# Kernel tuning notes

Measured on AMD Instinct MI355X. Metric: run time of the kernel, lower is better.

## Reference

```python
import jax, jax.numpy as jnp
import numpy as np

N = 100000
IN_CH = 1024
Z = 32
E = 1600000


def _gcn_conv(x, src, dst, W, b, n_nodes):
    # PyG GCNConv: add self-loops, symmetric deg^{-1/2} normalization,
    # message = norm * (x @ W)[src], scatter-add into dst, plus bias.
    loop = jnp.arange(n_nodes)
    s = jnp.concatenate([src, loop])
    d = jnp.concatenate([dst, loop])
    deg = jax.ops.segment_sum(jnp.ones_like(s, dtype=x.dtype), d, num_segments=n_nodes)
    dinv = jnp.where(deg > 0, jax.lax.rsqrt(deg), 0.0)
    norm = dinv[s] * dinv[d]                     # [E+N]
    h = x @ W                                    # [N, out]
    msg = h[s] * norm[:, None]                   # [E+N, out]
    out = jax.ops.segment_sum(msg, d, num_segments=n_nodes)
    return out + b


def setup_inputs() -> dict:
    key = jax.random.key(0)
    ks = jax.random.split(key, 10)
    x = jax.random.normal(ks[0], (N, IN_CH), dtype=jnp.float32)
    edge_index = jax.random.randint(ks[1], (2, E), 0, N, dtype=jnp.int64)
    def lin(k, fan_in, fan_out):
        bound = 1.0 / np.sqrt(fan_in)
        kw, kb = jax.random.split(k)
        W = jax.random.uniform(kw, (fan_in, fan_out), jnp.float32, -bound, bound)
        b = jax.random.uniform(kb, (fan_out,), jnp.float32, -bound, bound)
        return W, b
    Wg1, bg1 = lin(ks[2], IN_CH, 2 * Z)
    Wg2, bg2 = lin(ks[3], 2 * Z, Z)
    Wf1, bf1 = lin(ks[4], Z, 2 * Z)
    Wf2, bf2 = lin(ks[5], 2 * Z, IN_CH)
    return {"x": x, "edge_index": edge_index,
            "Wg1": Wg1, "bg1": bg1, "Wg2": Wg2, "bg2": bg2,
            "Wf1": Wf1, "bf1": bf1, "Wf2": Wf2, "bf2": bf2}


def reference(x, edge_index, Wg1, bg1, Wg2, bg2, Wf1, bf1, Wf2, bf2):
    src, dst = edge_index[0], edge_index[1]
    h = jax.nn.relu(_gcn_conv(x, src, dst, Wg1, bg1, N))
    z = _gcn_conv(h, src, dst, Wg2, bg2, N)          # encode output
    d = jax.nn.relu(z @ Wf1 + bf1)
    out = jax.nn.relu(d @ Wf2 + bf2)                 # decode output
    return out
```

## Files before the change

### kernel.cpp

```cpp
#include <hip/hip_runtime.h>

#define NN 100000
#define EE 1600000

using bf16x8 = __attribute__((ext_vector_type(8))) short;
using f32x4  = __attribute__((ext_vector_type(4))) float;

static __device__ __forceinline__ unsigned short f2bh(float f) {
    unsigned int u = __float_as_uint(f);
    return (unsigned short)((u + 0x7FFFu + ((u >> 16) & 1u)) >> 16);
}
static __device__ __forceinline__ float bh2f(unsigned short h) {
    return __uint_as_float(((unsigned int)h) << 16);
}

static __device__ __forceinline__ void split_pack(float4 a, float4 b,
                                                  bf16x8& h, bf16x8& l) {
    float f[8] = {a.x, a.y, a.z, a.w, b.x, b.y, b.z, b.w};
    union { bf16x8 v; unsigned int u[4]; } H, L;
    #pragma unroll
    for (int e = 0; e < 4; ++e) {
        unsigned int u0 = __float_as_uint(f[2 * e]);
        unsigned int u1 = __float_as_uint(f[2 * e + 1]);
        H.u[e] = (u0 >> 16) | (u1 & 0xFFFF0000u);
        float r0 = f[2 * e]     - __uint_as_float(u0 & 0xFFFF0000u);
        float r1 = f[2 * e + 1] - __uint_as_float(u1 & 0xFFFF0000u);
        L.u[e] = (__float_as_uint(r0) >> 16) | (__float_as_uint(r1) & 0xFFFF0000u);
    }
    h = H.v; l = L.v;
}

__global__ __launch_bounds__(256) void k_init(unsigned int* cursor) {
    int v = blockIdx.x * 256 + threadIdx.x;
    if (v < NN) cursor[v] = 0u;
}

__global__ __launch_bounds__(256) void k_fill(const int* __restrict__ src,
        const int* __restrict__ dst, unsigned int* cursor, int* __restrict__ bkt) {
    int e = blockIdx.x * 256 + threadIdx.x;
    if (e < EE) {
        int d = dst[e];
        unsigned int pos = atomicAdd(&cursor[d], 1u);
        bkt[(size_t)d * 64 + pos] = src[e];
    }
}

__global__ __launch_bounds__(256) void k_dinv(const unsigned int* __restrict__ deg, float* dinv) {
    int v = blockIdx.x * 256 + threadIdx.x;
    if (v < NN) dinv[v] = rsqrtf((float)(deg[v] + 1u));
}

__global__ __launch_bounds__(256) void k_prepW1(const float* __restrict__ W,
        unsigned short* __restrict__ img) {
    int t = blockIdx.x * 256 + threadIdx.x;
    int k = t >> 6, c = t & 63;
    float f = W[k * 64 + c];
    unsigned short h = f2bh(f);
    int chunk = k >> 5, kk = k & 31;
    size_t base = (size_t)chunk * 4608 + (size_t)c * 36 + kk;
    img[base] = h;
    img[base + 2304] = f2bh(f - bh2f(h));
}

__global__ __launch_bounds__(256) void k_prepW2(const float* __restrict__ W,
        unsigned short* __restrict__ wh, unsigned short* __restrict__ wl) {
    int t = blockIdx.x * 256 + threadIdx.x;
    int k = t >> 10, c = t & 1023;
    float f = W[k * 1024 + c];
    unsigned short h = f2bh(f);
    wh[c * 64 + k] = h;
    wl[c * 64 + k] = f2bh(f - bh2f(h));
}

__global__ __launch_bounds__(256) void k_gemm1(const float* __restrict__ x,
        const unsigned short* __restrict__ wimg,
        const float* __restrict__ dinv, float* __restrict__ g1) {
    __shared__ __align__(16) unsigned short bs[2][2][64][36];
    const int tid = threadIdx.x;
    const int lane = tid & 63, w = tid >> 6;
    const int l16 = lane & 15, g = lane >> 4;
    const int row0 = blockIdx.x * 64;
    const int rA = row0 + w * 16 + l16;
    const bool okA = rA < NN;
    const float* xp = x + (size_t)rA * 1024 + g * 8;
    const char* wb = (const char*)wimg;
    f32x4 acc[4] = {};
    for (int j = w; j < 9; j += 4)
        __builtin_amdgcn_global_load_lds((const unsigned int*)(wb + j * 1024 + lane * 16),
                                         (unsigned int*)((char*)&bs[0][0][0][0] + j * 1024), 16, 0, 0);
    float4 xr0 = make_float4(0.f,0.f,0.f,0.f), xr1 = xr0;
    if (okA) { xr0 = *(const float4*)(xp); xr1 = *(const float4*)(xp + 4); }
    __syncthreads();
    int cur = 0;
    for (int t = 0; t < 32; ++t) {
        float4 nx0 = make_float4(0.f,0.f,0.f,0.f), nx1 = nx0;
        if (t < 31) {
            const char* gb = wb + (size_t)(t + 1) * 9216;
            char* lb = (char*)&bs[cur ^ 1][0][0][0];
            for (int j = w; j < 9; j += 4)
                __builtin_amdgcn_global_load_lds((const unsigned int*)(gb + j * 1024 + lane * 16),
                                                 (unsigned int*)(lb + j * 1024), 16, 0, 0);
            if (okA) { nx0 = *(const float4*)(xp + (t + 1) * 32);
                       nx1 = *(const float4*)(xp + (t + 1) * 32 + 4); }
        }
        bf16x8 ah, al;
        split_pack(xr0, xr1, ah, al);
        #pragma unroll
        for (int nf = 0; nf < 4; ++nf) {
            bf16x8 bh = *(const bf16x8*)&bs[cur][0][nf * 16 + l16][g * 8];
            bf16x8 bl = *(const bf16x8*)&bs[cur][1][nf * 16 + l16][g * 8];
            acc[nf] = __builtin_amdgcn_mfma_f32_16x16x32_bf16(ah, bh, acc[nf], 0, 0, 0);
            acc[nf] = __builtin_amdgcn_mfma_f32_16x16x32_bf16(al, bh, acc[nf], 0, 0, 0);
            acc[nf] = __builtin_amdgcn_mfma_f32_16x16x32_bf16(ah, bl, acc[nf], 0, 0, 0);
        }
        __syncthreads();
        xr0 = nx0; xr1 = nx1; cur ^= 1;
    }
    #pragma unroll
    for (int r = 0; r < 4; ++r) {
        int node = row0 + w * 16 + g * 4 + r;
        if (node < NN) {
            float di = dinv[node];
            #pragma unroll
            for (int nf = 0; nf < 4; ++nf)
                g1[(size_t)node * 64 + nf * 16 + l16] = acc[nf][r] * di;
        }
    }
}

__global__ __launch_bounds__(256) void k_gather64(const float* __restrict__ g1,
        const int* __restrict__ bkt, const unsigned int* __restrict__ deg,
        const float* __restrict__ dinv, const float* __restrict__ bg1,
        float* __restrict__ h) {
    int wv = (blockIdx.x * 256 + threadIdx.x) >> 6;
    int lane = threadIdx.x & 63;
    if (wv >= NN) return;
    unsigned int n = deg[wv];
    const int* b = bkt + (size_t)wv * 64;
    float sum = g1[(size_t)wv * 64 + lane];
    unsigned int i = 0;
    for (; i + 4 <= n; i += 4) {
        int s0 = b[i], s1 = b[i + 1], s2 = b[i + 2], s3 = b[i + 3];
        float v0 = g1[(size_t)s0 * 64 + lane];
        float v1 = g1[(size_t)s1 * 64 + lane];
        float v2 = g1[(size_t)s2 * 64 + lane];
        float v3 = g1[(size_t)s3 * 64 + lane];
        sum += (v0 + v1) + (v2 + v3);
    }
    for (; i < n; ++i) sum += g1[(size_t)b[i] * 64 + lane];
    h[(size_t)wv * 64 + lane] = fmaxf(sum * dinv[wv] + bg1[lane], 0.f);
}

__global__ __launch_bounds__(256) void k_layer2(const float* __restrict__ h,
        const float* __restrict__ Wg2, const float* __restrict__ dinv,
        float* __restrict__ g2) {
    __shared__ __align__(16) float as[64][68];
    __shared__ __align__(16) float wsh[64][32];
    const int tid = threadIdx.x;
    const int node0 = blockIdx.x * 64;
    {
        const int lr = tid >> 4, lk = (tid & 15) * 4;
        #pragma unroll
        for (int l = 0; l < 4; ++l) {
            int r = lr + l * 16, v = node0 + r;
            float4 a = make_float4(0.f, 0.f, 0.f, 0.f);
            if (v < NN) a = *(const float4*)(h + (size_t)v * 64 + lk);
            *(float4*)&as[r][lk] = a;
        }
        const int wr = tid >> 3, wk = (tid & 7) * 4;
        #pragma unroll
        for (int l = 0; l < 2; ++l) {
            int r = wr + l * 32;
            *(float4*)&wsh[r][wk] = *(const float4*)(Wg2 + (size_t)r * 32 + wk);
        }
    }
    __syncthreads();
    const int tx = tid & 7, ty = tid >> 3;
    float acc[2][4] = {{0.f}};
    for (int kk = 0; kk < 64; kk += 4) {
        float wv[4][4];
        #pragma unroll
        for (int j = 0; j < 4; ++j)
            *(float4*)&wv[j][0] = *(const float4*)&wsh[kk + j][tx * 4];
        #pragma unroll
        for (int i = 0; i < 2; ++i) {
            float xv[4];
            *(float4*)&xv[0] = *(const float4*)&as[ty * 2 + i][kk];
            #pragma unroll
            for (int j = 0; j < 4; ++j) {
                #pragma unroll
                for (int c = 0; c < 4; ++c)
                    acc[i][c] += xv[j] * wv[j][c];
            }
        }
    }
    #pragma unroll
    for (int i = 0; i < 2; ++i) {
        int v = node0 + ty * 2 + i;
        if (v < NN) {
            float di = dinv[v];
            float4 o;
            o.x = acc[i][0] * di; o.y = acc[i][1] * di;
            o.z = acc[i][2] * di; o.w = acc[i][3] * di;
            *(float4*)(g2 + (size_t)v * 32 + tx * 4) = o;
        }
    }
}

__global__ __launch_bounds__(256) void k_gather32(const float* __restrict__ g2,
        const int* __restrict__ bkt, const unsigned int* __restrict__ deg,
        const float* __restrict__ dinv, const float* __restrict__ bg2,
        float* __restrict__ z) {
    int node = (blockIdx.x * 256 + threadIdx.x) >> 5;
    int c = threadIdx.x & 31;
    if (node >= NN) return;
    unsigned int n = deg[node];
    const int* b = bkt + (size_t)node * 64;
    float sum = g2[(size_t)node * 32 + c];
    unsigned int i = 0;
    for (; i + 4 <= n; i += 4) {
        int s0 = b[i], s1 = b[i + 1], s2 = b[i + 2], s3 = b[i + 3];
        float v0 = g2[(size_t)s0 * 32 + c];
        float v1 = g2[(size_t)s1 * 32 + c];
        float v2 = g2[(size_t)s2 * 32 + c];
        float v3 = g2[(size_t)s3 * 32 + c];
        sum += (v0 + v1) + (v2 + v3);
    }
    for (; i < n; ++i) sum += g2[(size_t)b[i] * 32 + c];
    z[(size_t)node * 32 + c] = sum * dinv[node] + bg2[c];
}

__global__ __launch_bounds__(256) void k_decode(const float* __restrict__ z,
        const float* __restrict__ Wf1, const float* __restrict__ bf1,
        const unsigned short* __restrict__ w2hg, const unsigned short* __restrict__ w2lg,
        const float* __restrict__ bf2, float* __restrict__ out) {
    __shared__ __align__(16) unsigned char smem[35328];
    float (*dsh)[68] = (float (*)[68])smem;
    float (*zs)[36]  = (float (*)[36])(smem + 17408);
    float (*w1s)[64] = (float (*)[64])(smem + 26624);
    unsigned short (*w2h)[72] = (unsigned short (*)[72])smem;
    unsigned short (*w2l)[72] = (unsigned short (*)[72])(smem + 9216);
    float (*ost)[66] = (float (*)[66])(smem + 18432);
    const int tid = threadIdx.x;
    const int lane = tid & 63, w = tid >> 6;
    const int l16 = lane & 15, g = lane >> 4;
    const int node0 = blockIdx.x * 64;

    uint4 ph[2], pl[2];
    #pragma unroll
    for (int j = 0; j < 2; ++j) {
        int fi = tid + 256 * j;
        int c = fi >> 3, k8 = (fi & 7) * 8;
        ph[j] = *(const uint4*)(w2hg + (size_t)c * 64 + k8);
        pl[j] = *(const uint4*)(w2lg + (size_t)c * 64 + k8);
    }

    #pragma unroll
    for (int j = 0; j < 2; ++j) {
        int fi = tid + 256 * j;
        int v = fi >> 3, m4 = (fi & 7) * 4;
        float4 zz = make_float4(0.f, 0.f, 0.f, 0.f);
        if (node0 + v < NN) zz = *(const float4*)(z + (size_t)(node0 + v) * 32 + m4);
        *(float4*)&zs[v][m4] = zz;
    }
    #pragma unroll
    for (int j = 0; j < 2; ++j) {
        int fi = tid + 256 * j;
        int r = fi >> 4, c4 = (fi & 15) * 4;
        *(float4*)&w1s[r][c4] = *(const float4*)(Wf1 + (size_t)r * 64 + c4);
    }
    __syncthreads();

    {
        const int dtx = tid & 15, dty = tid >> 4;
        float acc[4][4] = {{0.f}};
        for (int m = 0; m < 32; m += 4) {
            float wv[4][4];
            #pragma unroll
            for (int j = 0; j < 4; ++j)
                *(float4*)&wv[j][0] = *(const float4*)&w1s[m + j][dtx * 4];
            #pragma unroll
            for (int i = 0; i < 4; ++i) {
                float zv[4];
                *(float4*)&zv[0] = *(const float4*)&zs[dty * 4 + i][m];
                #pragma unroll
                for (int j = 0; j < 4; ++j) {
                    #pragma unroll
                    for (int c = 0; c < 4; ++c)
                        acc[i][c] += zv[j] * wv[j][c];
                }
            }
        }
        float4 b4 = *(const float4*)(bf1 + dtx * 4);
        #pragma unroll
        for (int i = 0; i < 4; ++i) {
            float4 dd;
            dd.x = fmaxf(acc[i][0] + b4.x, 0.f);
            dd.y = fmaxf(acc[i][1] + b4.y, 0.f);
            dd.z = fmaxf(acc[i][2] + b4.z, 0.f);
            dd.w = fmaxf(acc[i][3] + b4.w, 0.f);
            *(float4*)&dsh[dty * 4 + i][dtx * 4] = dd;
        }
    }
    __syncthreads();

    bf16x8 ah[2], al[2];
    {
        int row = w * 16 + l16;
        #pragma unroll
        for (int s = 0; s < 2; ++s) {
            int k0 = s * 32 + g * 8;
            float4 f0 = *(float4*)&dsh[row][k0];
            float4 f1 = *(float4*)&dsh[row][k0 + 4];
            float fv[8] = {f0.x, f0.y, f0.z, f0.w, f1.x, f1.y, f1.z, f1.w};
            bf16x8 hv, lv;
            #pragma unroll
            for (int e = 0; e < 8; ++e) {
                unsigned short hh = f2bh(fv[e]);
                hv[e] = (short)hh;
                lv[e] = (short)f2bh(fv[e] - bh2f(hh));
            }
            ah[s] = hv; al[s] = lv;
        }
    }
    __syncthreads();

    #pragma unroll
    for (int j = 0; j < 2; ++j) {
        int fi = tid + 256 * j;
        int c = fi >> 3, k8 = (fi & 7) * 8;
        *(uint4*)&w2h[c][k8] = ph[j];
        *(uint4*)&w2l[c][k8] = pl[j];
        ph[j] = *(const uint4*)(w2hg + (size_t)(64 + c) * 64 + k8);
        pl[j] = *(const uint4*)(w2lg + (size_t)(64 + c) * 64 + k8);
    }
    __syncthreads();

    for (int ch = 0; ch < 16; ++ch) {
        const int col0 = ch * 64;
        f32x4 acc[4] = {};
        #pragma unroll
        for (int nf = 0; nf < 4; ++nf) {
            int c = nf * 16 + l16;
            #pragma unroll
            for (int s = 0; s < 2; ++s) {
                int k0 = s * 32 + g * 8;
                bf16x8 bh = *(const bf16x8*)&w2h[c][k0];
                bf16x8 bl = *(const bf16x8*)&w2l[c][k0];
                acc[nf] = __builtin_amdgcn_mfma_f32_16x16x32_bf16(ah[s], bh, acc[nf], 0, 0, 0);
                acc[nf] = __builtin_amdgcn_mfma_f32_16x16x32_bf16(al[s], bh, acc[nf], 0, 0, 0);
                acc[nf] = __builtin_amdgcn_mfma_f32_16x16x32_bf16(ah[s], bl, acc[nf], 0, 0, 0);
            }
        }
        #pragma unroll
        for (int nf = 0; nf < 4; ++nf) {
            float b = bf2[col0 + nf * 16 + l16];
            #pragma unroll
            for (int r = 0; r < 4; ++r)
                ost[w * 16 + g * 4 + r][nf * 16 + l16] = fmaxf(acc[nf][r] + b, 0.f);
        }
        __syncthreads();
        if (ch < 15) {
            #pragma unroll
            for (int j = 0; j < 2; ++j) {
                int fi = tid + 256 * j;
                int c = fi >> 3, k8 = (fi & 7) * 8;
                *(uint4*)&w2h[c][k8] = ph[j];
                *(uint4*)&w2l[c][k8] = pl[j];
                if (ch < 14) {
                    ph[j] = *(const uint4*)(w2hg + (size_t)((ch + 2) * 64 + c) * 64 + k8);
                    pl[j] = *(const uint4*)(w2lg + (size_t)((ch + 2) * 64 + c) * 64 + k8);
                }
            }
        }
        #pragma unroll
        for (int j = 0; j < 4; ++j) {
            int fi = tid + 256 * j;
            int row = fi >> 4, c4 = (fi & 15) * 4;
            int node = node0 + row;
            if (node < NN) {
                float4 o = *(float4*)&ost[row][c4];
                *(float4*)(out + (size_t)node * 1024 + col0 + c4) = o;
            }
        }
        __syncthreads();
    }
}

extern "C" void kernel_launch(void* const* d_in, const int* in_sizes, int n_in,
                              void* d_out, int out_size, void* d_ws, size_t ws_size,
                              hipStream_t stream) {
    const float* x   = (const float*)d_in[0];
    const int* ei    = (const int*)d_in[1];
    const float* Wg1 = (const float*)d_in[2];
    const float* bg1 = (const float*)d_in[3];
    const float* Wg2 = (const float*)d_in[4];
    const float* bg2 = (const float*)d_in[5];
    const float* Wf1 = (const float*)d_in[6];
    const float* bf1 = (const float*)d_in[7];
    const float* Wf2 = (const float*)d_in[8];
    const float* bf2 = (const float*)d_in[9];
    float* out = (float*)d_out;
    float* ws  = (float*)d_ws;

    const int* src = ei;
    const int* dst = ei + EE;

    float* dinv = ws;
    float* g2   = ws + NN;
    float* z    = ws + NN + 32 * NN;
    unsigned short* wf2h = (unsigned short*)g2;
    unsigned short* wf2l = wf2h + 64 * 1024;

    float* g1 = out;
    float* h  = out + (size_t)64 * NN;
    int* bkt  = (int*)(out + (size_t)128 * NN);
    unsigned int* cursor = (unsigned int*)(bkt + (size_t)64 * NN);
    unsigned short* wg1img = (unsigned short*)(cursor + NN);

    k_init  <<<(NN + 255) / 256, 256, 0, stream>>>(cursor);
    k_fill  <<<(EE + 255) / 256, 256, 0, stream>>>(src, dst, cursor, bkt);
    k_dinv  <<<(NN + 255) / 256, 256, 0, stream>>>(cursor, dinv);
    k_prepW1<<<256, 256, 0, stream>>>(Wg1, wg1img);
    k_gemm1 <<<(NN + 63) / 64, 256, 0, stream>>>(x, wg1img, dinv, g1);
    k_gather64<<<(NN * 64 + 255) / 256, 256, 0, stream>>>(g1, bkt, cursor, dinv, bg1, h);
    k_layer2<<<(NN + 63) / 64, 256, 0, stream>>>(h, Wg2, dinv, g2);
    k_gather32<<<(NN * 32 + 255) / 256, 256, 0, stream>>>(g2, bkt, cursor, dinv, bg2, z);
    k_prepW2<<<256, 256, 0, stream>>>(Wf2, wf2h, wf2l);
    k_decode<<<(NN + 63) / 64, 256, 0, stream>>>(z, Wf1, bf1, wf2h, wf2l, bf2, out);
}
```

Measured before the change: 609.1 us.

## Load GEMM weights directly to registers, sort edge buckets, fuse prep kernels

The first GEMM now reads bf16 hi/lo weights straight from global memory into registers with software double-buffering. Each wave handles 32 rows, so a block covers 128 rows and there are no LDS stages or barriers. The decode kernel likewise reads Wf2 fragments from global memory, works on per-wave 32-column chunks and stages output per wave, dropping block-wide syncs. A new bitonic sort orders each node's neighbor list so gathers hit memory in ascending source order and summation order is deterministic, and W1 prep is fused with cursor init. The risk is extra redundant global and L2 weight traffic per wave, plus an added sort pass.

```diff
diff --git a/kernel.cpp b/kernel.cpp
--- a/kernel.cpp
+++ b/kernel.cpp
@@ -30,9 +30,19 @@
     h = H.v; l = L.v;
 }
 
-__global__ __launch_bounds__(256) void k_init(unsigned int* cursor) {
-    int v = blockIdx.x * 256 + threadIdx.x;
-    if (v < NN) cursor[v] = 0u;
+__global__ __launch_bounds__(256) void k_prep(const float* __restrict__ Wg1,
+        unsigned short* __restrict__ wg1h, unsigned short* __restrict__ wg1l,
+        unsigned int* __restrict__ cursor) {
+    int t = blockIdx.x * 256 + threadIdx.x;
+    if (t < 65536) {
+        int k = t >> 6, c = t & 63;
+        float f = Wg1[t];
+        unsigned short hh = f2bh(f);
+        wg1h[c * 1024 + k] = hh;
+        wg1l[c * 1024 + k] = f2bh(f - bh2f(hh));
+    } else if (t < 65536 + NN) {
+        cursor[t - 65536] = 0u;
+    }
 }
 
 __global__ __launch_bounds__(256) void k_fill(const int* __restrict__ src,
@@ -45,21 +55,28 @@
     }
 }
 
+__global__ __launch_bounds__(256) void k_sort(int* __restrict__ bkt,
+        const unsigned int* __restrict__ deg) {
+    int v = (blockIdx.x * 256 + threadIdx.x) >> 6;
+    int lane = threadIdx.x & 63;
+    if (v >= NN) return;
+    int n = (int)deg[v];
+    int val = (lane < n) ? bkt[(size_t)v * 64 + lane] : 0x7FFFFFFF;
+    #pragma unroll
+    for (int k = 2; k <= 64; k <<= 1) {
+        #pragma unroll
+        for (int j = k >> 1; j > 0; j >>= 1) {
+            int partner = __shfl_xor(val, j, 64);
+            bool takeMin = (((lane & k) == 0) == ((lane & j) == 0));
+            val = takeMin ? min(val, partner) : max(val, partner);
+        }
+    }
+    if (lane < n) bkt[(size_t)v * 64 + lane] = val;
+}
+
 __global__ __launch_bounds__(256) void k_dinv(const unsigned int* __restrict__ deg, float* dinv) {
     int v = blockIdx.x * 256 + threadIdx.x;
     if (v < NN) dinv[v] = rsqrtf((float)(deg[v] + 1u));
-}
-
-__global__ __launch_bounds__(256) void k_prepW1(const float* __restrict__ W,
-        unsigned short* __restrict__ img) {
-    int t = blockIdx.x * 256 + threadIdx.x;
-    int k = t >> 6, c = t & 63;
-    float f = W[k * 64 + c];
-    unsigned short h = f2bh(f);
-    int chunk = k >> 5, kk = k & 31;
-    size_t base = (size_t)chunk * 4608 + (size_t)c * 36 + kk;
-    img[base] = h;
-    img[base + 2304] = f2bh(f - bh2f(h));
 }
 
 __global__ __launch_bounds__(256) void k_prepW2(const float* __restrict__ W,
@@ -73,57 +90,68 @@
 }
 
 __global__ __launch_bounds__(256) void k_gemm1(const float* __restrict__ x,
-        const unsigned short* __restrict__ wimg,
+        const unsigned short* __restrict__ wh, const unsigned short* __restrict__ wl,
         const float* __restrict__ dinv, float* __restrict__ g1) {
-    __shared__ __align__(16) unsigned short bs[2][2][64][36];
     const int tid = threadIdx.x;
     const int lane = tid & 63, w = tid >> 6;
     const int l16 = lane & 15, g = lane >> 4;
-    const int row0 = blockIdx.x * 64;
-    const int rA = row0 + w * 16 + l16;
-    const bool okA = rA < NN;
-    const float* xp = x + (size_t)rA * 1024 + g * 8;
-    const char* wb = (const char*)wimg;
-    f32x4 acc[4] = {};
-    for (int j = w; j < 9; j += 4)
-        __builtin_amdgcn_global_load_lds((const unsigned int*)(wb + j * 1024 + lane * 16),
-                                         (unsigned int*)((char*)&bs[0][0][0][0] + j * 1024), 16, 0, 0);
-    float4 xr0 = make_float4(0.f,0.f,0.f,0.f), xr1 = xr0;
-    if (okA) { xr0 = *(const float4*)(xp); xr1 = *(const float4*)(xp + 4); }
-    __syncthreads();
-    int cur = 0;
-    for (int t = 0; t < 32; ++t) {
-        float4 nx0 = make_float4(0.f,0.f,0.f,0.f), nx1 = nx0;
-        if (t < 31) {
-            const char* gb = wb + (size_t)(t + 1) * 9216;
-            char* lb = (char*)&bs[cur ^ 1][0][0][0];
-            for (int j = w; j < 9; j += 4)
-                __builtin_amdgcn_global_load_lds((const unsigned int*)(gb + j * 1024 + lane * 16),
-                                                 (unsigned int*)(lb + j * 1024), 16, 0, 0);
-            if (okA) { nx0 = *(const float4*)(xp + (t + 1) * 32);
-                       nx1 = *(const float4*)(xp + (t + 1) * 32 + 4); }
-        }
-        bf16x8 ah, al;
-        split_pack(xr0, xr1, ah, al);
+    const int row0 = blockIdx.x * 128 + w * 32;
+    const int rA0 = row0 + l16, rA1 = row0 + 16 + l16;
+    const bool ok0 = rA0 < NN, ok1 = rA1 < NN;
+    const float* xp0 = x + (size_t)rA0 * 1024 + g * 8;
+    const float* xp1 = x + (size_t)rA1 * 1024 + g * 8;
+    const unsigned short* bhp = wh + (size_t)l16 * 1024 + g * 8;
+    const unsigned short* blp = wl + (size_t)l16 * 1024 + g * 8;
+    const float4 f40 = make_float4(0.f, 0.f, 0.f, 0.f);
+    f32x4 acc[2][4] = {};
+
+    auto loadt = [&](int t, bf16x8 bh[4], bf16x8 bl[4], float4 xv[4]) {
+        const int k0 = t * 32;
         #pragma unroll
         for (int nf = 0; nf < 4; ++nf) {
-            bf16x8 bh = *(const bf16x8*)&bs[cur][0][nf * 16 + l16][g * 8];
-            bf16x8 bl = *(const bf16x8*)&bs[cur][1][nf * 16 + l16][g * 8];
-            acc[nf] = __builtin_amdgcn_mfma_f32_16x16x32_bf16(ah, bh, acc[nf], 0, 0, 0);
-            acc[nf] = __builtin_amdgcn_mfma_f32_16x16x32_bf16(al, bh, acc[nf], 0, 0, 0);
-            acc[nf] = __builtin_amdgcn_mfma_f32_16x16x32_bf16(ah, bl, acc[nf], 0, 0, 0);
-        }
-        __syncthreads();
-        xr0 = nx0; xr1 = nx1; cur ^= 1;
-    }
-    #pragma unroll
-    for (int r = 0; r < 4; ++r) {
-        int node = row0 + w * 16 + g * 4 + r;
-        if (node < NN) {
-            float di = dinv[node];
-            #pragma unroll
-            for (int nf = 0; nf < 4; ++nf)
-                g1[(size_t)node * 64 + nf * 16 + l16] = acc[nf][r] * di;
+            bh[nf] = *(const bf16x8*)(bhp + (size_t)nf * 16384 + k0);
+            bl[nf] = *(const bf16x8*)(blp + (size_t)nf * 16384 + k0);
+        }
+        xv[0] = ok0 ? *(const float4*)(xp0 + k0)     : f40;
+        xv[1] = ok0 ? *(const float4*)(xp0 + k0 + 4) : f40;
+        xv[2] = ok1 ? *(const float4*)(xp1 + k0)     : f40;
+        xv[3] = ok1 ? *(const float4*)(xp1 + k0 + 4) : f40;
+    };
+    auto compute = [&](bf16x8 bh[4], bf16x8 bl[4], float4 xv[4]) {
+        bf16x8 ah0, al0, ah1, al1;
+        split_pack(xv[0], xv[1], ah0, al0);
+        split_pack(xv[2], xv[3], ah1, al1);
+        #pragma unroll
+        for (int nf = 0; nf < 4; ++nf) {
+            acc[0][nf] = __builtin_amdgcn_mfma_f32_16x16x32_bf16(ah0, bh[nf], acc[0][nf], 0, 0, 0);
+            acc[1][nf] = __builtin_amdgcn_mfma_f32_16x16x32_bf16(ah1, bh[nf], acc[1][nf], 0, 0, 0);
+            acc[0][nf] = __builtin_amdgcn_mfma_f32_16x16x32_bf16(al0, bh[nf], acc[0][nf], 0, 0, 0);
+            acc[1][nf] = __builtin_amdgcn_mfma_f32_16x16x32_bf16(al1, bh[nf], acc[1][nf], 0, 0, 0);
+            acc[0][nf] = __builtin_amdgcn_mfma_f32_16x16x32_bf16(ah0, bl[nf], acc[0][nf], 0, 0, 0);
+            acc[1][nf] = __builtin_amdgcn_mfma_f32_16x16x32_bf16(ah1, bl[nf], acc[1][nf], 0, 0, 0);
+        }
+    };
+
+    bf16x8 bhA[4], blA[4], bhB[4], blB[4];
+    float4 xA[4], xB[4];
+    loadt(0, bhA, blA, xA);
+    for (int t = 0; t < 32; t += 2) {
+        loadt(t + 1, bhB, blB, xB);
+        compute(bhA, blA, xA);
+        if (t + 2 < 32) loadt(t + 2, bhA, blA, xA);
+        compute(bhB, blB, xB);
+    }
+    #pragma unroll
+    for (int mf = 0; mf < 2; ++mf) {
+        #pragma unroll
+        for (int r = 0; r < 4; ++r) {
+            int node = row0 + mf * 16 + g * 4 + r;
+            if (node < NN) {
+                float di = dinv[node];
+                #pragma unroll
+                for (int nf = 0; nf < 4; ++nf)
+                    g1[(size_t)node * 64 + nf * 16 + l16] = acc[mf][nf][r] * di;
+            }
         }
     }
 }
@@ -234,26 +262,14 @@
         const float* __restrict__ Wf1, const float* __restrict__ bf1,
         const unsigned short* __restrict__ w2hg, const unsigned short* __restrict__ w2lg,
         const float* __restrict__ bf2, float* __restrict__ out) {
-    __shared__ __align__(16) unsigned char smem[35328];
+    __shared__ __align__(16) unsigned char smem[34816];
     float (*dsh)[68] = (float (*)[68])smem;
     float (*zs)[36]  = (float (*)[36])(smem + 17408);
     float (*w1s)[64] = (float (*)[64])(smem + 26624);
-    unsigned short (*w2h)[72] = (unsigned short (*)[72])smem;
-    unsigned short (*w2l)[72] = (unsigned short (*)[72])(smem + 9216);
-    float (*ost)[66] = (float (*)[66])(smem + 18432);
     const int tid = threadIdx.x;
     const int lane = tid & 63, w = tid >> 6;
     const int l16 = lane & 15, g = lane >> 4;
     const int node0 = blockIdx.x * 64;
-
-    uint4 ph[2], pl[2];
-    #pragma unroll
-    for (int j = 0; j < 2; ++j) {
-        int fi = tid + 256 * j;
-        int c = fi >> 3, k8 = (fi & 7) * 8;
-        ph[j] = *(const uint4*)(w2hg + (size_t)c * 64 + k8);
-        pl[j] = *(const uint4*)(w2lg + (size_t)c * 64 + k8);
-    }
 
     #pragma unroll
     for (int j = 0; j < 2; ++j) {
@@ -325,65 +341,52 @@
     }
     __syncthreads();
 
-    #pragma unroll
-    for (int j = 0; j < 2; ++j) {
-        int fi = tid + 256 * j;
-        int c = fi >> 3, k8 = (fi & 7) * 8;
-        *(uint4*)&w2h[c][k8] = ph[j];
-        *(uint4*)&w2l[c][k8] = pl[j];
-        ph[j] = *(const uint4*)(w2hg + (size_t)(64 + c) * 64 + k8);
-        pl[j] = *(const uint4*)(w2lg + (size_t)(64 + c) * 64 + k8);
-    }
-    __syncthreads();
-
-    for (int ch = 0; ch < 16; ++ch) {
-        const int col0 = ch * 64;
-        f32x4 acc[4] = {};
-        #pragma unroll
-        for (int nf = 0; nf < 4; ++nf) {
-            int c = nf * 16 + l16;
+    float (*ow)[34] = (float (*)[34])(smem + w * 2176);
+
+    auto loadw = [&](int ch, bf16x8 bh[2][2], bf16x8 bl[2][2]) {
+        #pragma unroll
+        for (int nf = 0; nf < 2; ++nf)
             #pragma unroll
             for (int s = 0; s < 2; ++s) {
-                int k0 = s * 32 + g * 8;
-                bf16x8 bh = *(const bf16x8*)&w2h[c][k0];
-                bf16x8 bl = *(const bf16x8*)&w2l[c][k0];
-                acc[nf] = __builtin_amdgcn_mfma_f32_16x16x32_bf16(ah[s], bh, acc[nf], 0, 0, 0);
-                acc[nf] = __builtin_amdgcn_mfma_f32_16x16x32_bf16(al[s], bh, acc[nf], 0, 0, 0);
-                acc[nf] = __builtin_amdgcn_mfma_f32_16x16x32_bf16(ah[s], bl, acc[nf], 0, 0, 0);
-            }
-        }
-        #pragma unroll
-        for (int nf = 0; nf < 4; ++nf) {
-            float b = bf2[col0 + nf * 16 + l16];
+                size_t off = (size_t)(ch * 32 + nf * 16 + l16) * 64 + s * 32 + g * 8;
+                bh[nf][s] = *(const bf16x8*)(w2hg + off);
+                bl[nf][s] = *(const bf16x8*)(w2lg + off);
+            }
+    };
+    auto dochunk = [&](int ch, bf16x8 bh[2][2], bf16x8 bl[2][2]) {
+        f32x4 acc[2] = {};
+        #pragma unroll
+        for (int nf = 0; nf < 2; ++nf)
+            #pragma unroll
+            for (int s = 0; s < 2; ++s) {
+                acc[nf] = __builtin_amdgcn_mfma_f32_16x16x32_bf16(ah[s], bh[nf][s], acc[nf], 0, 0, 0);
+                acc[nf] = __builtin_amdgcn_mfma_f32_16x16x32_bf16(al[s], bh[nf][s], acc[nf], 0, 0, 0);
+                acc[nf] = __builtin_amdgcn_mfma_f32_16x16x32_bf16(ah[s], bl[nf][s], acc[nf], 0, 0, 0);
+            }
+        #pragma unroll
+        for (int nf = 0; nf < 2; ++nf) {
+            float b = bf2[ch * 32 + nf * 16 + l16];
             #pragma unroll
             for (int r = 0; r < 4; ++r)
-                ost[w * 16 + g * 4 + r][nf * 16 + l16] = fmaxf(acc[nf][r] + b, 0.f);
-        }
-        __syncthreads();
-        if (ch < 15) {
-            #pragma unroll
-            for (int j = 0; j < 2; ++j) {
-                int fi = tid + 256 * j;
-                int c = fi >> 3, k8 = (fi & 7) * 8;
-                *(uint4*)&w2h[c][k8] = ph[j];
-                *(uint4*)&w2l[c][k8] = pl[j];
-                if (ch < 14) {
-                    ph[j] = *(const uint4*)(w2hg + (size_t)((ch + 2) * 64 + c) * 64 + k8);
-                    pl[j] = *(const uint4*)(w2lg + (size_t)((ch + 2) * 64 + c) * 64 + k8);
-                }
-            }
-        }
-        #pragma unroll
-        for (int j = 0; j < 4; ++j) {
-            int fi = tid + 256 * j;
-            int row = fi >> 4, c4 = (fi & 15) * 4;
-            int node = node0 + row;
-            if (node < NN) {
-                float4 o = *(float4*)&ost[row][c4];
-                *(float4*)(out + (size_t)node * 1024 + col0 + c4) = o;
-            }
-        }
-        __syncthreads();
+                ow[g * 4 + r][nf * 16 + l16] = fmaxf(acc[nf][r] + b, 0.f);
+        }
+        #pragma unroll
+        for (int i = 0; i < 2; ++i) {
+            int row = lane >> 2, q = (lane & 3) + 4 * i;
+            int node = node0 + w * 16 + row;
+            float4 o = *(float4*)&ow[row][q * 4];
+            if (node < NN)
+                *(float4*)(out + (size_t)node * 1024 + ch * 32 + q * 4) = o;
+        }
+    };
+
+    bf16x8 bhA[2][2], blA[2][2], bhB[2][2], blB[2][2];
+    loadw(0, bhA, blA);
+    for (int ch = 0; ch < 32; ch += 2) {
+        loadw(ch + 1, bhB, blB);
+        dochunk(ch, bhA, blA);
+        if (ch + 2 < 32) loadw(ch + 2, bhA, blA);
+        dochunk(ch + 1, bhB, blB);
     }
 }
 
@@ -416,13 +419,14 @@
     float* h  = out + (size_t)64 * NN;
     int* bkt  = (int*)(out + (size_t)128 * NN);
     unsigned int* cursor = (unsigned int*)(bkt + (size_t)64 * NN);
-    unsigned short* wg1img = (unsigned short*)(cursor + NN);
-
-    k_init  <<<(NN + 255) / 256, 256, 0, stream>>>(cursor);
+    unsigned short* wg1h = (unsigned short*)(cursor + NN);
+    unsigned short* wg1l = wg1h + 64 * 1024;
+
+    k_prep  <<<(65536 + NN + 255) / 256, 256, 0, stream>>>(Wg1, wg1h, wg1l, cursor);
     k_fill  <<<(EE + 255) / 256, 256, 0, stream>>>(src, dst, cursor, bkt);
+    k_sort  <<<(NN * 64 + 255) / 256, 256, 0, stream>>>(bkt, cursor);
     k_dinv  <<<(NN + 255) / 256, 256, 0, stream>>>(cursor, dinv);
-    k_prepW1<<<256, 256, 0, stream>>>(Wg1, wg1img);
-    k_gemm1 <<<(NN + 63) / 64, 256, 0, stream>>>(x, wg1img, dinv, g1);
+    k_gemm1 <<<(NN + 127) / 128, 256, 0, stream>>>(x, wg1h, wg1l, dinv, g1);
     k_gather64<<<(NN * 64 + 255) / 256, 256, 0, stream>>>(g1, bkt, cursor, dinv, bg1, h);
     k_layer2<<<(NN + 63) / 64, 256, 0, stream>>>(h, Wg2, dinv, g2);
     k_gather32<<<(NN * 32 + 255) / 256, 256, 0, stream>>>(g2, bkt, cursor, dinv, bg2, z);
```

After: 856.4 us. 1.41x slower.
